# Kernel tuning notes

Hardware: AMD Instinct MI355X
Metric: run time of the kernel (lower is better)

The kernel has to match this reference:

```python
import jax, jax.numpy as jnp
import numpy as np

HEAD_DIM = 64

def setup_inputs() -> dict:
    key = jax.random.key(0)
    k1, k2, k3, k4 = jax.random.split(key, 4)
    B, T, C, D = 8, 2048, 1024, HEAD_DIM
    x = jax.random.normal(k1, (B, T, C), dtype=jnp.float32)
    Wq = jax.random.normal(k2, (C, D), dtype=jnp.float32) * (1.0 / np.sqrt(C))
    Wk = jax.random.normal(k3, (C, D), dtype=jnp.float32) * (1.0 / np.sqrt(C))
    Wv = jax.random.normal(k4, (C, D), dtype=jnp.float32) * (1.0 / np.sqrt(C))
    return {"x": x, "Wq": Wq, "Wk": Wk, "Wv": Wv}

def reference(x, Wq, Wk, Wv):
    B, T, C = x.shape
    D = Wq.shape[1]
    q = jnp.einsum('btc,cd->btd', x, Wq)
    k = jnp.einsum('btc,cd->btd', x, Wk)
    v = jnp.einsum('btc,cd->btd', x, Wv)
    scale = 1.0 / jnp.sqrt(jnp.asarray(D, dtype=x.dtype))
    wei = jnp.einsum('bqd,bkd->bqk', q, k) * scale  # [B,T,T]
    causal = jnp.tril(jnp.ones((T, T), dtype=bool))
    wei = jnp.where(causal[None, :, :], wei, -jnp.inf)
    wei = jax.nn.softmax(wei, axis=-1)
    # dropout p=0.0 (eval) -> identity
    out = jnp.einsum('bqk,bkd->bqd', wei, v)  # [B,T,D]
    return out
```

## Files before the change

### kernel.cpp

```cpp
#include <hip/hip_runtime.h>
#include <hip/hip_bf16.h>


typedef __attribute__((ext_vector_type(8))) short short8;
typedef __attribute__((ext_vector_type(4))) float f32x4;

#define MFMA16(a, b, c) __builtin_amdgcn_mfma_f32_16x16x32_bf16((a), (b), (c), 0, 0, 0)

__device__ __forceinline__ unsigned short f2bf(float f) {
  unsigned int u = __builtin_bit_cast(unsigned int, f);
  unsigned int r = 0x7fffu + ((u >> 16) & 1u);
  return (unsigned short)((u + r) >> 16);
}
__device__ __forceinline__ float bf2f(unsigned short h) {
  unsigned int u = ((unsigned int)h) << 16;
  return __builtin_bit_cast(float, u);
}

#define BATCH 8
#define SEQ   2048
#define CDIM  1024
#define DDIM  64
#define NTOK  (BATCH * SEQ)
#define LOG2E 1.44269504f

__global__ __launch_bounds__(256) void wt_kernel(const float* __restrict__ Wq,
                                                 const float* __restrict__ Wk,
                                                 const float* __restrict__ Wv,
                                                 unsigned short* __restrict__ WT) {
  int tid = blockIdx.x * 256 + threadIdx.x;
  int c    = tid & 63;
  int rest = tid >> 6;
  int k    = rest & 1023;
  int wi   = rest >> 10;
  const float* W = (wi == 0) ? Wq : ((wi == 1) ? Wk : Wv);
  float v = W[k * DDIM + c];
  if (wi == 0) v *= 0.125f * LOG2E;
  int row  = wi * 64 + c;
  int step = k >> 6;
  int col  = k & 63;
  size_t idx = (size_t)step * 12288 + (size_t)row * 64 +
               (size_t)(((col >> 3) ^ (row & 7)) * 8) + (col & 7);
  WT[idx] = f2bf(v);
}

__global__ __launch_bounds__(512) void proj_kernel(const float* __restrict__ x,
                                                   const unsigned short* __restrict__ WT,
                                                   unsigned short* __restrict__ qws,
                                                   unsigned short* __restrict__ kws,
                                                   unsigned short* __restrict__ vtws) {
  __shared__ __align__(16) unsigned short xs[2][32 * 64];
  __shared__ __align__(16) unsigned short wl[2][192 * 64];

  const int tid  = threadIdx.x;
  const int lane = tid & 63;
  const int w    = tid >> 6;
  const int wm   = w & 1;
  const int wn   = w >> 1;
  const int c16  = lane & 15;
  const int hi   = lane >> 4;
  const int id   = blockIdx.x;
  const int n0   = (id & 7) * SEQ + (id >> 3) * 32;
  const bool xldr = (tid < 256);
  const int trow = (tid >> 3) & 31;
  const int kch  = tid & 7;

  f32x4 acc[3];
#pragma unroll
  for (int ct = 0; ct < 3; ++ct) acc[ct] = (f32x4){0.f, 0.f, 0.f, 0.f};

  const float* xbase = x + (size_t)(n0 + trow) * CDIM + kch * 8;
  const int xsw = trow * 64 + ((kch ^ (trow & 7)) * 8);

  const unsigned short* wsrc = WT + (size_t)w * 1536 + (size_t)lane * 8;
  auto stage_wt = [&](int step, int bufi) {
    const unsigned short* s = wsrc + (size_t)step * 12288;
    unsigned short* d = &wl[bufi][w * 1536];
#pragma unroll
    for (int j = 0; j < 3; ++j)
      __builtin_amdgcn_global_load_lds(
          (const __attribute__((address_space(1))) void*)(s + j * 512),
          (__attribute__((address_space(3))) void*)(d + j * 512), 16, 0, 0);
  };
  auto xstore = [&](f32x4 a, f32x4 b, int bufi) {
    short8 h;
#pragma unroll
    for (int j = 0; j < 4; ++j) { h[j] = (short)f2bf(a[j]); h[4 + j] = (short)f2bf(b[j]); }
    *reinterpret_cast<short8*>(&xs[bufi][xsw]) = h;
  };

  f32x4 xa1 = {0,0,0,0}, xb1 = xa1, xa2 = xa1, xb2 = xa1;
  if (xldr) {
    f32x4 a0 = *reinterpret_cast<const f32x4*>(xbase);
    f32x4 b0 = *reinterpret_cast<const f32x4*>(xbase + 4);
    xstore(a0, b0, 0);
    xa1 = *reinterpret_cast<const f32x4*>(xbase + 64);
    xb1 = *reinterpret_cast<const f32x4*>(xbase + 64 + 4);
  }
  stage_wt(0, 0);
  __syncthreads();

  int cur = 0;
  for (int st = 0; st < 16; ++st) {
    if (st + 2 < 16 && xldr) {
      xa2 = *reinterpret_cast<const f32x4*>(xbase + (st + 2) * 64);
      xb2 = *reinterpret_cast<const f32x4*>(xbase + (st + 2) * 64 + 4);
    }
    if (st + 1 < 16) stage_wt(st + 1, cur ^ 1);

    short8 bfrag[2];
    {
      int r = wm * 16 + c16;
#pragma unroll
      for (int f = 0; f < 2; ++f)
        bfrag[f] = *reinterpret_cast<const short8*>(
            &xs[cur][r * 64 + (((f * 4 + hi) ^ (r & 7)) * 8)]);
    }
#pragma unroll
    for (int ct = 0; ct < 3; ++ct) {
      int ra = (wn * 3 + ct) * 16 + c16;
#pragma unroll
      for (int f = 0; f < 2; ++f) {
        short8 af = *reinterpret_cast<const short8*>(
            &wl[cur][ra * 64 + (((f * 4 + hi) ^ (ra & 7)) * 8)]);
        acc[ct] = MFMA16(af, bfrag[f], acc[ct]);
      }
    }

    if (st + 1 < 16 && xldr) xstore(xa1, xb1, cur ^ 1);
    __syncthreads();
    xa1 = xa2; xb1 = xb2;
    cur ^= 1;
  }

  {
    const int token = n0 + wm * 16 + c16;
    const int b = token >> 11;
    const int t = token & 2047;
#pragma unroll
    for (int ct = 0; ct < 3; ++ct) {
      int cg = (wn * 3 + ct) * 16 + hi * 4;
      unsigned short h[4];
#pragma unroll
      for (int r = 0; r < 4; ++r) h[r] = f2bf(acc[ct][r]);
      if (cg < 64) {
        *reinterpret_cast<ushort4*>(qws + (size_t)token * DDIM + cg) =
            make_ushort4(h[0], h[1], h[2], h[3]);
      } else if (cg < 128) {
        *reinterpret_cast<ushort4*>(kws + (size_t)token * DDIM + (cg - 64)) =
            make_ushort4(h[0], h[1], h[2], h[3]);
      } else {
        int cv = cg - 128;
#pragma unroll
        for (int r = 0; r < 4; ++r)
          vtws[(size_t)(b * DDIM + cv + r) * SEQ + t] = h[r];
      }
    }
  }
}

__global__ __launch_bounds__(256) void attn_partial(const unsigned short* __restrict__ qws,
                                                    const unsigned short* __restrict__ kws,
                                                    const unsigned short* __restrict__ vtws,
                                                    unsigned short* __restrict__ po,
                                                    float* __restrict__ pml,
                                                    int MAXCH, int CHUNK) {
  __shared__ __align__(16) unsigned short kt[2][64 * 64];
  __shared__ __align__(16) unsigned short vt[2][64 * 64];
  __shared__ __align__(16) unsigned short pt[4][1024];

  const int id = blockIdx.x;
  const int b  = id & 7;
  const int qt = (id >> 3) & 31;
  const int ch = id >> 8;

  const int kv_end = qt * 64 + 64;
  const int kv0_ch = ch * CHUNK;
  if (kv0_ch >= kv_end) return;
  const int block_lim = min(kv0_ch + CHUNK, kv_end);
  const int nt = (block_lim - kv0_ch + 63) >> 6;

  const int tid  = threadIdx.x;
  const int lane = tid & 63;
  const int w    = tid >> 6;
  const int c    = lane & 15;
  const int hi   = lane >> 4;
  const int qr0  = qt * 64 + w * 16;
  const int q    = qr0 + c;
  const int kv_last = qr0 + 15;

  const unsigned short* qb = qws + (size_t)b * SEQ * DDIM;
  short8 aq0 = *reinterpret_cast<const short8*>(qb + (size_t)q * DDIM + hi * 8);
  short8 aq1 = *reinterpret_cast<const short8*>(qb + (size_t)q * DDIM + 32 + hi * 8);

  float m = -INFINITY, l = 0.f;
  f32x4 o[4];
#pragma unroll
  for (int dn = 0; dn < 4; ++dn) o[dn] = (f32x4){0.f, 0.f, 0.f, 0.f};

  unsigned short* pwv = pt[w];
  const unsigned short* kb = kws + (size_t)b * SEQ * DDIM;
  const unsigned short* vb = vtws + (size_t)b * DDIM * SEQ;

  auto stage_kv = [&](int bufi, int kv0) {
#pragma unroll
    for (int j = 0; j < 2; ++j) {
      int p   = w * 128 + j * 64 + lane;
      int row = p >> 3;
      int chk = (p & 7) ^ (row & 7);
      __builtin_amdgcn_global_load_lds(
          (const __attribute__((address_space(1))) void*)(kb + (size_t)(kv0 + row) * DDIM + chk * 8),
          (__attribute__((address_space(3))) void*)(&kt[bufi][w * 1024 + j * 512]), 16, 0, 0);
      __builtin_amdgcn_global_load_lds(
          (const __attribute__((address_space(1))) void*)(vb + (size_t)row * SEQ + kv0 + chk * 8),
          (__attribute__((address_space(3))) void*)(&vt[bufi][w * 1024 + j * 512]), 16, 0, 0);
    }
  };

  stage_kv(0, kv0_ch);
  asm volatile("s_waitcnt vmcnt(0)" ::: "memory");
  __builtin_amdgcn_s_barrier();

  int cur = 0;
  for (int t = 0; t < nt; ++t) {
    const int kv0 = kv0_ch + t * 64;
    if (t + 1 < nt) stage_kv(cur ^ 1, kv0 + 64);

    if (kv0 <= kv_last) {
      f32x4 s[4];
#pragma unroll
      for (int n = 0; n < 4; ++n) {
        if (kv0 + n * 16 > kv_last) {
          s[n] = (f32x4){-INFINITY, -INFINITY, -INFINITY, -INFINITY};
          continue;
        }
        const unsigned short* kr = &kt[cur][(n * 16 + c) * 64];
        short8 ka0 = *reinterpret_cast<const short8*>(kr + ((hi ^ (c & 7)) * 8));
        short8 ka1 = *reinterpret_cast<const short8*>(kr + (((4 + hi) ^ (c & 7)) * 8));
        f32x4 z = (f32x4){0.f, 0.f, 0.f, 0.f};
        z = MFMA16(ka0, aq0, z);
        s[n] = MFMA16(ka1, aq1, z);
      }

      if (kv0 + 63 > qr0) {
#pragma unroll
        for (int n = 0; n < 4; ++n)
#pragma unroll
          for (int r = 0; r < 4; ++r)
            if (kv0 + n * 16 + hi * 4 + r > q) s[n][r] = -INFINITY;
      }

      float mx = -INFINITY;
#pragma unroll
      for (int n = 0; n < 4; ++n)
        mx = fmaxf(mx, fmaxf(fmaxf(s[n][0], s[n][1]), fmaxf(s[n][2], s[n][3])));
      mx = fmaxf(mx, __shfl_xor(mx, 16, 64));
      mx = fmaxf(mx, __shfl_xor(mx, 32, 64));

      float nm = fmaxf(m, mx);
      float sc = __builtin_exp2f(m - nm);
      m = nm;

      float ssum = 0.f;
#pragma unroll
      for (int n = 0; n < 4; ++n) {
        float pv0 = __builtin_exp2f(s[n][0] - nm);
        float pv1 = __builtin_exp2f(s[n][1] - nm);
        float pv2 = __builtin_exp2f(s[n][2] - nm);
        float pv3 = __builtin_exp2f(s[n][3] - nm);
        ssum += (pv0 + pv1) + (pv2 + pv3);
        ushort4 h4 = make_ushort4(f2bf(pv0), f2bf(pv1), f2bf(pv2), f2bf(pv3));
        *reinterpret_cast<ushort4*>(
            pwv + (2 * n + (hi >> 1)) * 128 + c * 8 + (hi & 1) * 4) = h4;
      }
      ssum += __shfl_xor(ssum, 16, 64);
      ssum += __shfl_xor(ssum, 32, 64);
      l = l * sc + ssum;

#pragma unroll
      for (int dn = 0; dn < 4; ++dn) o[dn] *= sc;

      const int nf = (kv0 + 32 <= kv_last) ? 2 : 1;
      for (int f = 0; f < nf; ++f) {
        short8 bp = *reinterpret_cast<const short8*>(pwv + (f * 4 + hi) * 128 + c * 8);
#pragma unroll
        for (int dn = 0; dn < 4; ++dn) {
          const unsigned short* vr = &vt[cur][(dn * 16 + c) * 64];
          short8 va = *reinterpret_cast<const short8*>(vr + (((f * 4 + hi) ^ (c & 7)) * 8));
          o[dn] = MFMA16(va, bp, o[dn]);
        }
      }
    }

    if (t + 1 < nt) {
      asm volatile("s_waitcnt vmcnt(0)" ::: "memory");
      __builtin_amdgcn_s_barrier();
    }
    cur ^= 1;
  }

  unsigned short* pob =
      po + (((size_t)(b * 32 + qt) * MAXCH + ch) * 64 + w * 16 + c) * 64 + hi * 4;
#pragma unroll
  for (int dn = 0; dn < 4; ++dn) {
    ushort4 h4 = make_ushort4(f2bf(o[dn][0]), f2bf(o[dn][1]),
                              f2bf(o[dn][2]), f2bf(o[dn][3]));
    *reinterpret_cast<ushort4*>(pob + dn * 16) = h4;
  }

  if (hi == 0) {
    *reinterpret_cast<float2*>(
        pml + (((size_t)(b * 32 + qt) * MAXCH + ch) * 64 + w * 16 + c) * 2) =
        make_float2(m, l);
  }
}

__global__ __launch_bounds__(256) void attn_combine(const unsigned short* __restrict__ po,
                                                    const float* __restrict__ pml,
                                                    float* __restrict__ out,
                                                    int MAXCH, int CHUNK) {
  const int id = blockIdx.x;
  const int b  = id & 7;
  const int qt = id >> 3;
  const int tid = threadIdx.x;
  const int row = tid >> 2;
  const int cg  = tid & 3;
  const int nch = min((qt * 64 + 64 + CHUNK - 1) / CHUNK, MAXCH);

  const size_t base = (size_t)(b * 32 + qt) * MAXCH;

  float mv0 = -INFINITY, mv1 = -INFINITY, mv2 = -INFINITY, mv3 = -INFINITY;
  float mv4 = -INFINITY, mv5 = -INFINITY, mv6 = -INFINITY, mv7 = -INFINITY;
  float lv0 = 0, lv1 = 0, lv2 = 0, lv3 = 0, lv4 = 0, lv5 = 0, lv6 = 0, lv7 = 0;
#define LOADML(i) if (i < nch) { \
    float2 t = *reinterpret_cast<const float2*>(pml + (base + i) * 128 + row * 2); \
    mv##i = t.x; lv##i = t.y; }
  LOADML(0) LOADML(1) LOADML(2) LOADML(3) LOADML(4) LOADML(5) LOADML(6) LOADML(7)
#undef LOADML

  float M = fmaxf(fmaxf(fmaxf(mv0, mv1), fmaxf(mv2, mv3)),
                  fmaxf(fmaxf(mv4, mv5), fmaxf(mv6, mv7)));

  float L = 0.f;
  f32x4 a0 = {0.f,0.f,0.f,0.f}, a1 = a0, a2 = a0, a3 = a0;
#define ACC(i) if (i < nch) { \
    float wgt = __builtin_exp2f(mv##i - M); \
    L += wgt * lv##i; \
    const unsigned short* p = po + (base + i) * 4096 + row * 64 + cg * 16; \
    short8 v0 = *reinterpret_cast<const short8*>(p); \
    short8 v1 = *reinterpret_cast<const short8*>(p + 8); \
    f32x4 t0, t1, t2, t3; \
    for (int j = 0; j < 4; ++j) { \
      t0[j] = bf2f((unsigned short)v0[j]); \
      t1[j] = bf2f((unsigned short)v0[4 + j]); \
      t2[j] = bf2f((unsigned short)v1[j]); \
      t3[j] = bf2f((unsigned short)v1[4 + j]); \
    } \
    a0 += wgt * t0; a1 += wgt * t1; a2 += wgt * t2; a3 += wgt * t3; }
  ACC(0) ACC(1) ACC(2) ACC(3) ACC(4) ACC(5) ACC(6) ACC(7)
#undef ACC

  float invL = 1.f / L;
  float* ob = out + ((size_t)b * SEQ + qt * 64 + row) * 64 + cg * 16;
  *reinterpret_cast<f32x4*>(ob)      = a0 * invL;
  *reinterpret_cast<f32x4*>(ob + 4)  = a1 * invL;
  *reinterpret_cast<f32x4*>(ob + 8)  = a2 * invL;
  *reinterpret_cast<f32x4*>(ob + 12) = a3 * invL;
}

extern "C" void kernel_launch(void* const* d_in, const int* in_sizes, int n_in,
                              void* d_out, int out_size, void* d_ws, size_t ws_size,
                              hipStream_t stream) {
  const float* x  = (const float*)d_in[0];
  const float* Wq = (const float*)d_in[1];
  const float* Wk = (const float*)d_in[2];
  const float* Wv = (const float*)d_in[3];
  float* out = (float*)d_out;

  unsigned short* qws  = (unsigned short*)d_ws;
  unsigned short* kws  = qws + (size_t)NTOK * DDIM;
  unsigned short* vtws = kws + (size_t)NTOK * DDIM;
  unsigned short* WT   = vtws + (size_t)NTOK * DDIM;
  size_t fixed_end = (size_t)NTOK * DDIM * 3 * 2 + 192 * 1024 * 2;

  int MAXCH = 1;
  {
    const int cand[4] = {8, 4, 2, 1};
    for (int i = 0; i < 4; ++i) {
      size_t need = fixed_end +
                    (size_t)cand[i] * (8ull * 32 * 64 * 64 * 2 + 8ull * 32 * 64 * 2 * 4);
      if (need <= ws_size) { MAXCH = cand[i]; break; }
    }
  }

  wt_kernel<<<768, 256, 0, stream>>>(Wq, Wk, Wv, WT);
  proj_kernel<<<NTOK / 32, 512, 0, stream>>>(x, WT, qws, kws, vtws);

  unsigned short* po = (unsigned short*)((char*)d_ws + fixed_end);
  float* pml = (float*)(po + (size_t)BATCH * 32 * MAXCH * 64 * 64);
  int CHUNK = SEQ / MAXCH;
  attn_partial<<<32 * MAXCH * BATCH, 256, 0, stream>>>(qws, kws, vtws, po, pml,
                                                       MAXCH, CHUNK);
  attn_combine<<<32 * BATCH, 256, 0, stream>>>(po, pml, out, MAXCH, CHUNK);
}
```

Baseline: 53.77 us.

## Fuse split-KV combine into partial kernel via last-block atomic counter

Removes the separate combine kernel launch. Each split-KV partial block fences its writes and atomically increments a per-(batch,query-tile) counter, and the last-arriving block performs the log-sum-exp merge and writes the final output. This saves a kernel launch and its tail, at the cost of an extra memset launch, atomics, and a serialized combine inside the final block of each tile.

Result: slower. 214.3 us (+298.5%).

```diff
diff --git a/kernel.cpp b/kernel.cpp
--- a/kernel.cpp
+++ b/kernel.cpp
@@ -164,6 +164,8 @@
                                                     const unsigned short* __restrict__ vtws,
                                                     unsigned short* __restrict__ po,
                                                     float* __restrict__ pml,
+                                                    float* __restrict__ out,
+                                                    unsigned int* __restrict__ cnt,
                                                     int MAXCH, int CHUNK) {
   __shared__ __align__(16) unsigned short kt[2][64 * 64];
   __shared__ __align__(16) unsigned short vt[2][64 * 64];
@@ -179,6 +181,7 @@
   if (kv0_ch >= kv_end) return;
   const int block_lim = min(kv0_ch + CHUNK, kv_end);
   const int nt = (block_lim - kv0_ch + 63) >> 6;
+  const int nch = min((kv_end + CHUNK - 1) / CHUNK, MAXCH);
 
   const int tid  = threadIdx.x;
   const int lane = tid & 63;
@@ -313,59 +316,61 @@
         pml + (((size_t)(b * 32 + qt) * MAXCH + ch) * 64 + w * 16 + c) * 2) =
         make_float2(m, l);
   }
-}
-
-__global__ __launch_bounds__(256) void attn_combine(const unsigned short* __restrict__ po,
-                                                    const float* __restrict__ pml,
-                                                    float* __restrict__ out,
-                                                    int MAXCH, int CHUNK) {
-  const int id = blockIdx.x;
-  const int b  = id & 7;
-  const int qt = id >> 3;
-  const int tid = threadIdx.x;
-  const int row = tid >> 2;
-  const int cg  = tid & 3;
-  const int nch = min((qt * 64 + 64 + CHUNK - 1) / CHUNK, MAXCH);
-
-  const size_t base = (size_t)(b * 32 + qt) * MAXCH;
-
-  float mv0 = -INFINITY, mv1 = -INFINITY, mv2 = -INFINITY, mv3 = -INFINITY;
-  float mv4 = -INFINITY, mv5 = -INFINITY, mv6 = -INFINITY, mv7 = -INFINITY;
-  float lv0 = 0, lv1 = 0, lv2 = 0, lv3 = 0, lv4 = 0, lv5 = 0, lv6 = 0, lv7 = 0;
+
+  __threadfence();
+  __syncthreads();
+  __shared__ int lastflag;
+  if (tid == 0) {
+    unsigned int old = atomicAdd(&cnt[b * 32 + qt], 1u);
+    lastflag = (old == (unsigned int)(nch - 1));
+  }
+  __syncthreads();
+  if (!lastflag) return;
+  __threadfence();
+
+  {
+    const int row = tid >> 2;
+    const int cg  = tid & 3;
+    const size_t base = (size_t)(b * 32 + qt) * MAXCH;
+
+    float mv0 = -INFINITY, mv1 = -INFINITY, mv2 = -INFINITY, mv3 = -INFINITY;
+    float mv4 = -INFINITY, mv5 = -INFINITY, mv6 = -INFINITY, mv7 = -INFINITY;
+    float lv0 = 0, lv1 = 0, lv2 = 0, lv3 = 0, lv4 = 0, lv5 = 0, lv6 = 0, lv7 = 0;
 #define LOADML(i) if (i < nch) { \
-    float2 t = *reinterpret_cast<const float2*>(pml + (base + i) * 128 + row * 2); \
-    mv##i = t.x; lv##i = t.y; }
-  LOADML(0) LOADML(1) LOADML(2) LOADML(3) LOADML(4) LOADML(5) LOADML(6) LOADML(7)
+      float2 t2 = *reinterpret_cast<const float2*>(pml + (base + i) * 128 + row * 2); \
+      mv##i = t2.x; lv##i = t2.y; }
+    LOADML(0) LOADML(1) LOADML(2) LOADML(3) LOADML(4) LOADML(5) LOADML(6) LOADML(7)
 #undef LOADML
 
-  float M = fmaxf(fmaxf(fmaxf(mv0, mv1), fmaxf(mv2, mv3)),
-                  fmaxf(fmaxf(mv4, mv5), fmaxf(mv6, mv7)));
-
-  float L = 0.f;
-  f32x4 a0 = {0.f,0.f,0.f,0.f}, a1 = a0, a2 = a0, a3 = a0;
+    float M = fmaxf(fmaxf(fmaxf(mv0, mv1), fmaxf(mv2, mv3)),
+                    fmaxf(fmaxf(mv4, mv5), fmaxf(mv6, mv7)));
+
+    float L = 0.f;
+    f32x4 a0 = {0.f,0.f,0.f,0.f}, a1 = a0, a2 = a0, a3 = a0;
 #define ACC(i) if (i < nch) { \
-    float wgt = __builtin_exp2f(mv##i - M); \
-    L += wgt * lv##i; \
-    const unsigned short* p = po + (base + i) * 4096 + row * 64 + cg * 16; \
-    short8 v0 = *reinterpret_cast<const short8*>(p); \
-    short8 v1 = *reinterpret_cast<const short8*>(p + 8); \
-    f32x4 t0, t1, t2, t3; \
-    for (int j = 0; j < 4; ++j) { \
-      t0[j] = bf2f((unsigned short)v0[j]); \
-      t1[j] = bf2f((unsigned short)v0[4 + j]); \
-      t2[j] = bf2f((unsigned short)v1[j]); \
-      t3[j] = bf2f((unsigned short)v1[4 + j]); \
-    } \
-    a0 += wgt * t0; a1 += wgt * t1; a2 += wgt * t2; a3 += wgt * t3; }
-  ACC(0) ACC(1) ACC(2) ACC(3) ACC(4) ACC(5) ACC(6) ACC(7)
+      float wgt = __builtin_exp2f(mv##i - M); \
+      L += wgt * lv##i; \
+      const unsigned short* p = po + (base + i) * 4096 + row * 64 + cg * 16; \
+      short8 v0 = *reinterpret_cast<const short8*>(p); \
+      short8 v1 = *reinterpret_cast<const short8*>(p + 8); \
+      f32x4 t0, t1, t2, t3; \
+      for (int j = 0; j < 4; ++j) { \
+        t0[j] = bf2f((unsigned short)v0[j]); \
+        t1[j] = bf2f((unsigned short)v0[4 + j]); \
+        t2[j] = bf2f((unsigned short)v1[j]); \
+        t3[j] = bf2f((unsigned short)v1[4 + j]); \
+      } \
+      a0 += wgt * t0; a1 += wgt * t1; a2 += wgt * t2; a3 += wgt * t3; }
+    ACC(0) ACC(1) ACC(2) ACC(3) ACC(4) ACC(5) ACC(6) ACC(7)
 #undef ACC
 
-  float invL = 1.f / L;
-  float* ob = out + ((size_t)b * SEQ + qt * 64 + row) * 64 + cg * 16;
-  *reinterpret_cast<f32x4*>(ob)      = a0 * invL;
-  *reinterpret_cast<f32x4*>(ob + 4)  = a1 * invL;
-  *reinterpret_cast<f32x4*>(ob + 8)  = a2 * invL;
-  *reinterpret_cast<f32x4*>(ob + 12) = a3 * invL;
+    float invL = 1.f / L;
+    float* ob = out + ((size_t)b * SEQ + qt * 64 + row) * 64 + cg * 16;
+    *reinterpret_cast<f32x4*>(ob)      = a0 * invL;
+    *reinterpret_cast<f32x4*>(ob + 4)  = a1 * invL;
+    *reinterpret_cast<f32x4*>(ob + 8)  = a2 * invL;
+    *reinterpret_cast<f32x4*>(ob + 12) = a3 * invL;
+  }
 }
 
 extern "C" void kernel_launch(void* const* d_in, const int* in_sizes, int n_in,
@@ -387,7 +392,7 @@
   {
     const int cand[4] = {8, 4, 2, 1};
     for (int i = 0; i < 4; ++i) {
-      size_t need = fixed_end +
+      size_t need = fixed_end + 1024 +
                     (size_t)cand[i] * (8ull * 32 * 64 * 64 * 2 + 8ull * 32 * 64 * 2 * 4);
       if (need <= ws_size) { MAXCH = cand[i]; break; }
     }
@@ -398,8 +403,10 @@
 
   unsigned short* po = (unsigned short*)((char*)d_ws + fixed_end);
   float* pml = (float*)(po + (size_t)BATCH * 32 * MAXCH * 64 * 64);
+  unsigned int* cnt = (unsigned int*)(pml + (size_t)BATCH * 32 * MAXCH * 64 * 2);
   int CHUNK = SEQ / MAXCH;
+
+  hipMemsetAsync(cnt, 0, 256 * sizeof(unsigned int), stream);
   attn_partial<<<32 * MAXCH * BATCH, 256, 0, stream>>>(qws, kws, vtws, po, pml,
-                                                       MAXCH, CHUNK);
-  attn_combine<<<32 * BATCH, 256, 0, stream>>>(po, pml, out, MAXCH, CHUNK);
-}
+                                                       out, cnt, MAXCH, CHUNK);
+}
```
